# Optimization experiments

Measured on AMD Instinct MI355X. Metric: run time of the kernel, lower is better.

The kernel has to match this reference:

```python
import jax, jax.numpy as jnp
import numpy as np

N = 8192       # num nodes
D_IN = 256     # in_features
D_OUT = 128    # out_features per head
H = 2          # num_heads
E = 262144     # num edges (avg degree 32)
ALPHA = 0.2    # leaky relu slope


def setup_inputs() -> dict:
    key = jax.random.key(0)
    k1, k2, k3, k4 = jax.random.split(key, 4)
    x = jax.random.normal(k1, (N, D_IN), dtype=jnp.float32)
    # per-head Linear weights: W[h] is [out, in] (y = x @ W.T), a[h] is [2*out]
    W = jax.random.normal(k2, (H, D_OUT, D_IN), dtype=jnp.float32) * (1.0 / np.sqrt(D_IN))
    a = jax.random.normal(k3, (H, 2 * D_OUT), dtype=jnp.float32) * (1.0 / np.sqrt(2 * D_OUT))
    edge_index = jax.random.randint(k4, (2, E), 0, N, dtype=jnp.int32)
    return {"x": x, "W": W, "a": a, "edge_index": edge_index}


def reference(x, W, a, edge_index):
    # h[h,n,d] = W(x) per head
    h = jnp.einsum('nf,hdf->hnd', x, W)
    # a([h_i ; h_j]) decomposes into a_src . h_i + a_dst . h_j
    a_src, a_dst = a[:, :D_OUT], a[:, D_OUT:]
    s_i = jnp.einsum('hnd,hd->hn', h, a_src)
    s_j = jnpp_dummy = None
    s_j = jnp.einsum('hnd,hd->hn', h, a_dst)
    score = s_i[:, :, None] + s_j[:, None, :]  # [H, n, n]
    # dense adjacency mask from edge list
    adj = jnp.zeros((N, N), dtype=jnp.bool_).at[edge_index[0], edge_index[1]].set(True)
    # faithful to original: non-edges set to 0 (NOT -inf) before leaky_relu + softmax
    e = jnp.where(adj[None, :, :], score, jnp.float32(0.0))
    e = jnp.where(e > 0, e, ALPHA * e)  # leaky relu
    att = jax.nn.softmax(e, axis=-1)    # softmax over j (dim=1 of original [n,n])
    out = jnp.einsum('hij,hjd->hid', att, h)  # aggregate: attention @ h
    out = jnp.transpose(out, (1, 0, 2)).reshape(N, H * D_OUT)  # concat heads
    return jax.nn.elu(out)
```

## Files before the change

kernel.cpp:

```cpp
#include <hip/hip_runtime.h>
#include <hip/hip_bf16.h>

#define N_NODES 8192
#define DIN     256
#define DOUT    128
#define NHEAD   2
#define CTOT    256
#define NWORDS  256
#define LRELU_A 0.2f
#define CAPN    128

typedef __attribute__((ext_vector_type(8))) short bf16x8;
typedef __attribute__((ext_vector_type(4))) float f32x4;

__device__ __forceinline__ float bf(unsigned short u) {
    return __uint_as_float((unsigned)u << 16);
}
__device__ __forceinline__ float bflo(unsigned u) { return __uint_as_float(u << 16); }
__device__ __forceinline__ float bfhi(unsigned u) { return __uint_as_float(u & 0xffff0000u); }
__device__ __forceinline__ unsigned short f2bf(float f) {
    unsigned u = __float_as_uint(f);
    u = (u + 0x7fffu + ((u >> 16) & 1u)) >> 16;
    return (unsigned short)u;
}
__device__ __forceinline__ unsigned pk(float a, float b) {
    return (unsigned)f2bf(a) | ((unsigned)f2bf(b) << 16);
}

__global__ __launch_bounds__(256) void k_pre(const float* __restrict__ x,
                                             const float* __restrict__ W,
                                             const float* __restrict__ a,
                                             unsigned short* __restrict__ hb16,
                                             float* __restrict__ sp_src,
                                             float* __restrict__ sp_dst,
                                             float* __restrict__ cpart,
                                             float4* __restrict__ adjp) {
    __shared__ unsigned short As[64 * 256];
    __shared__ unsigned short Bs[64 * 256];
    __shared__ float          cpl[4][64];
    int b = blockIdx.x, t = threadIdx.x;

    if (b >= 512) {
        adjp[(b - 512) * 256 + t] = make_float4(0.f, 0.f, 0.f, 0.f);
        return;
    }

    int bmi = b & 127;
    int bm = bmi * 64;
    int bn = (b >> 7) * 64;
    int wv = t >> 6, lane = t & 63;
    int fr = lane & 15, ksl = lane >> 4;

    #pragma unroll
    for (int i = 0; i < 16; ++i) {
        int idx = i * 256 + t;
        int row = idx >> 6;
        int kq  = (idx & 63) * 4;
        float4 v = *reinterpret_cast<const float4*>(&x[(bm + row) * DIN + kq]);
        int slot = kq >> 3, half = (kq >> 2) & 1;
        *reinterpret_cast<uint2*>(&As[row * 256 + ((slot ^ (row & 7)) << 3) + half * 4]) =
            make_uint2(pk(v.x, v.y), pk(v.z, v.w));
    }
    #pragma unroll
    for (int i = 0; i < 16; ++i) {
        int idx = i * 256 + t;
        int row = idx >> 6;
        int kq  = (idx & 63) * 4;
        float4 v = *reinterpret_cast<const float4*>(&W[(bn + row) * DIN + kq]);
        int slot = kq >> 3, half = (kq >> 2) & 1;
        *reinterpret_cast<uint2*>(&Bs[row * 256 + ((slot ^ (row & 7)) << 3) + half * 4]) =
            make_uint2(pk(v.x, v.y), pk(v.z, v.w));
    }
    __syncthreads();

    f32x4 acc[4] = {};
    #pragma unroll
    for (int ch = 0; ch < 8; ++ch) {
        int s = ch * 4 + ksl;
        int ra = wv * 16 + fr;
        bf16x8 af = *reinterpret_cast<const bf16x8*>(&As[ra * 256 + ((s ^ (ra & 7)) << 3)]);
        #pragma unroll
        for (int fn = 0; fn < 4; ++fn) {
            int rb = fn * 16 + fr;
            bf16x8 bfr = *reinterpret_cast<const bf16x8*>(&Bs[rb * 256 + ((s ^ (rb & 7)) << 3)]);
            acc[fn] = __builtin_amdgcn_mfma_f32_16x16x32_bf16(af, bfr, acc[fn], 0, 0, 0);
        }
    }

    #pragma unroll
    for (int fn = 0; fn < 4; ++fn) {
        int c = bn + fn * 16 + fr;
        int r0 = bm + wv * 16 + ksl * 4;
        #pragma unroll
        for (int r = 0; r < 4; ++r)
            hb16[(size_t)(r0 + r) * CTOT + c] = f2bf(acc[fn][r]);
    }

    #pragma unroll
    for (int fn = 0; fn < 4; ++fn) {
        float s = acc[fn][0] + acc[fn][1] + acc[fn][2] + acc[fn][3];
        s += __shfl_xor(s, 16);
        s += __shfl_xor(s, 32);
        if (ksl == 0) cpl[wv][fn * 16 + fr] = s;
    }
    __syncthreads();
    if (t < 64)
        cpart[bmi * 256 + bn + t] = cpl[0][t] + cpl[1][t] + cpl[2][t] + cpl[3][t];

    int head = (bn >= 128);
    int q    = bn >> 6;
    float as[4], ad[4];
    #pragma unroll
    for (int fn = 0; fn < 4; ++fn) {
        int d = (bn & 127) + fn * 16 + fr;
        as[fn] = a[head * 256 + d];
        ad[fn] = a[head * 256 + 128 + d];
    }
    #pragma unroll
    for (int r = 0; r < 4; ++r) {
        float ps = acc[0][r] * as[0] + acc[1][r] * as[1] + acc[2][r] * as[2] + acc[3][r] * as[3];
        float pd = acc[0][r] * ad[0] + acc[1][r] * ad[1] + acc[2][r] * ad[2] + acc[3][r] * ad[3];
        #pragma unroll
        for (int off = 8; off; off >>= 1) {
            ps += __shfl_xor(ps, off);
            pd += __shfl_xor(pd, off);
        }
        if (fr == 0) {
            int row = bm + wv * 16 + ksl * 4 + r;
            sp_src[q * N_NODES + row] = ps;
            sp_dst[q * N_NODES + row] = pd;
        }
    }
}

__global__ __launch_bounds__(256) void k_mid(const int* __restrict__ ei, int E,
                                             unsigned int* __restrict__ adjw,
                                             const float* __restrict__ sp_src,
                                             const float* __restrict__ sp_dst,
                                             const float* __restrict__ cpart,
                                             float* __restrict__ s_src,
                                             float* __restrict__ s_dst,
                                             float* __restrict__ S_all) {
    int b = blockIdx.x, t = threadIdx.x;

    if (b < 1024) {
        int e = b * 256 + t;
        if (e < E) {
            int src = ei[e];
            int dst = ei[E + e];
            atomicOr(&adjw[(size_t)src * NWORDS + (dst >> 5)], 1u << (dst & 31));
        }
        return;
    }
    if (b < 1056) {
        int n = (b - 1024) * 256 + t;
        s_src[n]           = sp_src[0 * N_NODES + n] + sp_src[1 * N_NODES + n];
        s_src[N_NODES + n] = sp_src[2 * N_NODES + n] + sp_src[3 * N_NODES + n];
        s_dst[n]           = sp_dst[0 * N_NODES + n] + sp_dst[1 * N_NODES + n];
        s_dst[N_NODES + n] = sp_dst[2 * N_NODES + n] + sp_dst[3 * N_NODES + n];
        return;
    }

    float s = 0.f;
    #pragma unroll 16
    for (int p = 0; p < 128; ++p)
        s += cpart[p * 256 + t];
    S_all[t] = s;
}

__global__ __launch_bounds__(256) void k_attn(const unsigned int* __restrict__ adjw,
                                              const float* __restrict__ s_src,
                                              const float* __restrict__ s_dst,
                                              const unsigned short* __restrict__ hb16,
                                              const float* __restrict__ S_all,
                                              float* __restrict__ out) {
    __shared__ unsigned short nbr[4][CAPN];
    __shared__ float          ewl[4][CAPN];
    __shared__ float          zr[4];
    __shared__ float4         part[4][64];

    int i    = blockIdx.x;
    int t    = threadIdx.x;
    int wv   = t >> 6;
    int lane = t & 63;
    int head = wv >> 1;

    const uint4 wq = reinterpret_cast<const uint4*>(adjw + (size_t)i * NWORDS)[lane];
    int cnt = __popc(wq.x) + __popc(wq.y) + __popc(wq.z) + __popc(wq.w);
    int inc = cnt;
    #pragma unroll
    for (int off = 1; off < 64; off <<= 1) {
        int v = __shfl_up(inc, off);
        if (lane >= off) inc += v;
    }
    int deg = __shfl(inc, 63);
    int pos = inc - cnt;
    int idb = lane * 128;
    {
        unsigned int w;
        w = wq.x; while (w) { int bb = __ffs(w) - 1; w &= w - 1; if (pos < CAPN) nbr[wv][pos] = (unsigned short)(idb + bb);      ++pos; }
        w = wq.y; while (w) { int bb = __ffs(w) - 1; w &= w - 1; if (pos < CAPN) nbr[wv][pos] = (unsigned short)(idb + 32 + bb); ++pos; }
        w = wq.z; while (w) { int bb = __ffs(w) - 1; w &= w - 1; if (pos < CAPN) nbr[wv][pos] = (unsigned short)(idb + 64 + bb); ++pos; }
        w = wq.w; while (w) { int bb = __ffs(w) - 1; w &= w - 1; if (pos < CAPN) nbr[wv][pos] = (unsigned short)(idb + 96 + bb); ++pos; }
    }
    if (deg > CAPN) deg = CAPN;

    float ssh = s_src[head * N_NODES + i];
    const float* sdh = s_dst + head * N_NODES;
    float z = 0.f;
    for (int k = lane; k < deg; k += 64) {
        int j = nbr[wv][k];
        float v = ssh + sdh[j];
        float e = v > 0.f ? v : LRELU_A * v;
        float w = expf(e) - 1.f;
        ewl[wv][k] = w;
        z += w;
    }
    #pragma unroll
    for (int off = 32; off; off >>= 1)
        z += __shfl_xor(z, off);
    if (lane == 0) zr[wv] = (float)N_NODES + z;
    __syncthreads();

    const uint2* hb2 = reinterpret_cast<const uint2*>(hb16);
    bool lo = lane < 32;
    float4 acc = make_float4(0.f, 0.f, 0.f, 0.f);
    int k = wv;
    for (; k + 28 < deg; k += 32) {
        int   jj[8]; float ww[8]; uint2 hv[8];
        #pragma unroll
        for (int u = 0; u < 8; ++u) {
            int kk = k + u * 4;
            jj[u] = nbr[wv][kk];
            ww[u] = lo ? ewl[0][kk] : ewl[2][kk];
            hv[u] = hb2[jj[u] * 64 + lane];
        }
        #pragma unroll
        for (int u = 0; u < 8; ++u) {
            acc.x = fmaf(ww[u], bflo(hv[u].x), acc.x);
            acc.y = fmaf(ww[u], bfhi(hv[u].x), acc.y);
            acc.z = fmaf(ww[u], bflo(hv[u].y), acc.z);
            acc.w = fmaf(ww[u], bfhi(hv[u].y), acc.w);
        }
    }
    for (; k < deg; k += 4) {
        int j = nbr[wv][k];
        float w = lo ? ewl[0][k] : ewl[2][k];
        uint2 hv = hb2[j * 64 + lane];
        acc.x = fmaf(w, bflo(hv.x), acc.x);
        acc.y = fmaf(w, bfhi(hv.x), acc.y);
        acc.z = fmaf(w, bflo(hv.y), acc.z);
        acc.w = fmaf(w, bfhi(hv.y), acc.w);
    }
    part[wv][lane] = acc;
    __syncthreads();

    if (t < 64) {
        float4 c0 = part[0][t], c1 = part[1][t], c2 = part[2][t], c3 = part[3][t];
        float4 s;
        s.x = c0.x + c1.x + c2.x + c3.x;
        s.y = c0.y + c1.y + c2.y + c3.y;
        s.z = c0.z + c1.z + c2.z + c3.z;
        s.w = c0.w + c1.w + c2.w + c3.w;
        float4 sa = reinterpret_cast<const float4*>(S_all)[t];
        float rz = 1.f / ((t >= 32) ? zr[2] : zr[0]);
        float4 o;
        o.x = (sa.x + s.x) * rz; o.y = (sa.y + s.y) * rz;
        o.z = (sa.z + s.z) * rz; o.w = (sa.w + s.w) * rz;
        o.x = o.x > 0.f ? o.x : expm1f(o.x);
        o.y = o.y > 0.f ? o.y : expm1f(o.y);
        o.z = o.z > 0.f ? o.z : expm1f(o.z);
        o.w = o.w > 0.f ? o.w : expm1f(o.w);
        reinterpret_cast<float4*>(out)[i * 64 + t] = o;
    }
}

extern "C" void kernel_launch(void* const* d_in, const int* in_sizes, int n_in,
                              void* d_out, int out_size, void* d_ws, size_t ws_size,
                              hipStream_t stream) {
    const float* x  = (const float*)d_in[0];
    const float* W  = (const float*)d_in[1];
    const float* a  = (const float*)d_in[2];
    const int*   ei = (const int*)d_in[3];
    int E = in_sizes[3] / 2;
    float* out = (float*)d_out;

    char* ws = (char*)d_ws;
    size_t off = 0;
    auto alloc = [&](size_t bytes) { char* p = ws + off; off += (bytes + 255) & ~(size_t)255; return p; };
    unsigned int*   adjw   = (unsigned int*)  alloc((size_t)N_NODES * NWORDS * 4);
    float*          S_all  = (float*)         alloc(CTOT * 4);
    float*          s_src  = (float*)         alloc((size_t)NHEAD * N_NODES * 4);
    float*          s_dst  = (float*)         alloc((size_t)NHEAD * N_NODES * 4);
    unsigned short* hb16   = (unsigned short*)alloc((size_t)N_NODES * CTOT * 2);
    float*          sp_src = (float*)         alloc((size_t)4 * N_NODES * 4);
    float*          sp_dst = (float*)         alloc((size_t)4 * N_NODES * 4);
    float*          cpart  = (float*)         alloc((size_t)128 * 256 * 4);

    k_pre<<<2560, 256, 0, stream>>>(x, W, a, hb16, sp_src, sp_dst, cpart, (float4*)adjw);
    k_mid<<<1057, 256, 0, stream>>>(ei, E, adjw, sp_src, sp_dst, cpart, s_src, s_dst, S_all);
    k_attn<<<N_NODES, 256, 0, stream>>>(adjw, s_src, s_dst, hb16, S_all, out);
}
```

Before: 55.07 us.

## Replace dense bitmask adjacency with atomic-count CSR neighbor lists

The dense 8192x8192 bit adjacency (8 MB zeroed and scanned per row) is replaced by per-node neighbor lists of capacity CAPN, filled by atomicAdd on a per-node count. The attention kernel reads the row directly instead of doing a popcount/prefix-scan compaction. It removes duplicate edges with a shared-memory bitmask and atomicOr, zeroing their weights. This cuts the zeroing traffic and the 1 KB-per-row bitmap reads, but adds contended global atomics. Neighbor order now depends on atomic order, so summation order is no longer deterministic.

Result: no change. 55.37 us (+0.5%).

```diff
diff --git a/kernel.cpp b/kernel.cpp
--- a/kernel.cpp
+++ b/kernel.cpp
@@ -6,7 +6,6 @@
 #define DOUT    128
 #define NHEAD   2
 #define CTOT    256
-#define NWORDS  256
 #define LRELU_A 0.2f
 #define CAPN    128
 
@@ -34,14 +33,17 @@
                                              float* __restrict__ sp_src,
                                              float* __restrict__ sp_dst,
                                              float* __restrict__ cpart,
-                                             float4* __restrict__ adjp) {
+                                             int*   __restrict__ cnt) {
     __shared__ unsigned short As[64 * 256];
     __shared__ unsigned short Bs[64 * 256];
     __shared__ float          cpl[4][64];
     int b = blockIdx.x, t = threadIdx.x;
 
-    if (b >= 512) {
-        adjp[(b - 512) * 256 + t] = make_float4(0.f, 0.f, 0.f, 0.f);
+    if (b == 512) {
+        int4* c4 = reinterpret_cast<int4*>(cnt);
+        #pragma unroll
+        for (int u = 0; u < 8; ++u)
+            c4[u * 256 + t] = make_int4(0, 0, 0, 0);
         return;
     }
 
@@ -134,7 +136,8 @@
 }
 
 __global__ __launch_bounds__(256) void k_mid(const int* __restrict__ ei, int E,
-                                             unsigned int* __restrict__ adjw,
+                                             int* __restrict__ cnt,
+                                             unsigned short* __restrict__ csr,
                                              const float* __restrict__ sp_src,
                                              const float* __restrict__ sp_dst,
                                              const float* __restrict__ cpart,
@@ -148,7 +151,9 @@
         if (e < E) {
             int src = ei[e];
             int dst = ei[E + e];
-            atomicOr(&adjw[(size_t)src * NWORDS + (dst >> 5)], 1u << (dst & 31));
+            int pos = atomicAdd(&cnt[src], 1);
+            if (pos < CAPN)
+                csr[(size_t)src * CAPN + pos] = (unsigned short)dst;
         }
         return;
     }
@@ -168,58 +173,52 @@
     S_all[t] = s;
 }
 
-__global__ __launch_bounds__(256) void k_attn(const unsigned int* __restrict__ adjw,
+__global__ __launch_bounds__(256) void k_attn(const int* __restrict__ cnt,
+                                              const unsigned short* __restrict__ csr,
                                               const float* __restrict__ s_src,
                                               const float* __restrict__ s_dst,
                                               const unsigned short* __restrict__ hb16,
                                               const float* __restrict__ S_all,
                                               float* __restrict__ out) {
-    __shared__ unsigned short nbr[4][CAPN];
-    __shared__ float          ewl[4][CAPN];
-    __shared__ float          zr[4];
-    __shared__ float4         part[4][64];
+    __shared__ unsigned mask[2][256];
+    __shared__ float    ewl[2][CAPN];
+    __shared__ float    zr[2];
+    __shared__ float4   part[4][64];
 
     int i    = blockIdx.x;
     int t    = threadIdx.x;
     int wv   = t >> 6;
     int lane = t & 63;
-    int head = wv >> 1;
-
-    const uint4 wq = reinterpret_cast<const uint4*>(adjw + (size_t)i * NWORDS)[lane];
-    int cnt = __popc(wq.x) + __popc(wq.y) + __popc(wq.z) + __popc(wq.w);
-    int inc = cnt;
-    #pragma unroll
-    for (int off = 1; off < 64; off <<= 1) {
-        int v = __shfl_up(inc, off);
-        if (lane >= off) inc += v;
-    }
-    int deg = __shfl(inc, 63);
-    int pos = inc - cnt;
-    int idb = lane * 128;
-    {
-        unsigned int w;
-        w = wq.x; while (w) { int bb = __ffs(w) - 1; w &= w - 1; if (pos < CAPN) nbr[wv][pos] = (unsigned short)(idb + bb);      ++pos; }
-        w = wq.y; while (w) { int bb = __ffs(w) - 1; w &= w - 1; if (pos < CAPN) nbr[wv][pos] = (unsigned short)(idb + 32 + bb); ++pos; }
-        w = wq.z; while (w) { int bb = __ffs(w) - 1; w &= w - 1; if (pos < CAPN) nbr[wv][pos] = (unsigned short)(idb + 64 + bb); ++pos; }
-        w = wq.w; while (w) { int bb = __ffs(w) - 1; w &= w - 1; if (pos < CAPN) nbr[wv][pos] = (unsigned short)(idb + 96 + bb); ++pos; }
-    }
+    int deg  = cnt[i];
     if (deg > CAPN) deg = CAPN;
-
-    float ssh = s_src[head * N_NODES + i];
-    const float* sdh = s_dst + head * N_NODES;
-    float z = 0.f;
-    for (int k = lane; k < deg; k += 64) {
-        int j = nbr[wv][k];
-        float v = ssh + sdh[j];
-        float e = v > 0.f ? v : LRELU_A * v;
-        float w = expf(e) - 1.f;
-        ewl[wv][k] = w;
-        z += w;
-    }
-    #pragma unroll
-    for (int off = 32; off; off >>= 1)
-        z += __shfl_xor(z, off);
-    if (lane == 0) zr[wv] = (float)N_NODES + z;
+    const unsigned short* row = csr + (size_t)i * CAPN;
+
+    if ((wv & 1) == 0) {
+        int hp = wv >> 1;
+        #pragma unroll
+        for (int u = 0; u < 4; ++u)
+            mask[hp][u * 64 + lane] = 0u;
+        float ssh = s_src[hp * N_NODES + i];
+        const float* sdh = s_dst + hp * N_NODES;
+        float z = 0.f;
+        for (int k = lane; k < deg; k += 64) {
+            int j = row[k];
+            unsigned bit = 1u << (j & 31);
+            unsigned old = atomicOr(&mask[hp][j >> 5], bit);
+            float w = 0.f;
+            if (!(old & bit)) {
+                float v = ssh + sdh[j];
+                float e = v > 0.f ? v : LRELU_A * v;
+                w = expf(e) - 1.f;
+            }
+            ewl[hp][k] = w;
+            z += w;
+        }
+        #pragma unroll
+        for (int off = 32; off; off >>= 1)
+            z += __shfl_xor(z, off);
+        if (lane == 0) zr[hp] = (float)N_NODES + z;
+    }
     __syncthreads();
 
     const uint2* hb2 = reinterpret_cast<const uint2*>(hb16);
@@ -231,8 +230,8 @@
         #pragma unroll
         for (int u = 0; u < 8; ++u) {
             int kk = k + u * 4;
-            jj[u] = nbr[wv][kk];
-            ww[u] = lo ? ewl[0][kk] : ewl[2][kk];
+            jj[u] = row[kk];
+            ww[u] = lo ? ewl[0][kk] : ewl[1][kk];
             hv[u] = hb2[jj[u] * 64 + lane];
         }
         #pragma unroll
@@ -244,8 +243,8 @@
         }
     }
     for (; k < deg; k += 4) {
-        int j = nbr[wv][k];
-        float w = lo ? ewl[0][k] : ewl[2][k];
+        int j = row[k];
+        float w = lo ? ewl[0][k] : ewl[1][k];
         uint2 hv = hb2[j * 64 + lane];
         acc.x = fmaf(w, bflo(hv.x), acc.x);
         acc.y = fmaf(w, bfhi(hv.x), acc.y);
@@ -263,7 +262,7 @@
         s.z = c0.z + c1.z + c2.z + c3.z;
         s.w = c0.w + c1.w + c2.w + c3.w;
         float4 sa = reinterpret_cast<const float4*>(S_all)[t];
-        float rz = 1.f / ((t >= 32) ? zr[2] : zr[0]);
+        float rz = 1.f / ((t >= 32) ? zr[1] : zr[0]);
         float4 o;
         o.x = (sa.x + s.x) * rz; o.y = (sa.y + s.y) * rz;
         o.z = (sa.z + s.z) * rz; o.w = (sa.w + s.w) * rz;
@@ -288,7 +287,8 @@
     char* ws = (char*)d_ws;
     size_t off = 0;
     auto alloc = [&](size_t bytes) { char* p = ws + off; off += (bytes + 255) & ~(size_t)255; return p; };
-    unsigned int*   adjw   = (unsigned int*)  alloc((size_t)N_NODES * NWORDS * 4);
+    int*            cnt    = (int*)           alloc((size_t)N_NODES * 4);
+    unsigned short* csr    = (unsigned short*)alloc((size_t)N_NODES * CAPN * 2);
     float*          S_all  = (float*)         alloc(CTOT * 4);
     float*          s_src  = (float*)         alloc((size_t)NHEAD * N_NODES * 4);
     float*          s_dst  = (float*)         alloc((size_t)NHEAD * N_NODES * 4);
@@ -297,7 +297,7 @@
     float*          sp_dst = (float*)         alloc((size_t)4 * N_NODES * 4);
     float*          cpart  = (float*)         alloc((size_t)128 * 256 * 4);
 
-    k_pre<<<2560, 256, 0, stream>>>(x, W, a, hb16, sp_src, sp_dst, cpart, (float4*)adjw);
-    k_mid<<<1057, 256, 0, stream>>>(ei, E, adjw, sp_src, sp_dst, cpart, s_src, s_dst, S_all);
-    k_attn<<<N_NODES, 256, 0, stream>>>(adjw, s_src, s_dst, hb16, S_all, out);
-}
+    k_pre<<<513, 256, 0, stream>>>(x, W, a, hb16, sp_src, sp_dst, cpart, cnt);
+    k_mid<<<1057, 256, 0, stream>>>(ei, E, cnt, csr, sp_src, sp_dst, cpart, s_src, s_dst, S_all);
+    k_attn<<<N_NODES, 256, 0, stream>>>(cnt, csr, s_src, s_dst, hb16, S_all, out);
+}
```
